# Kernel tuning notes

Hardware: AMD Instinct MI355X
Metric: run time of the kernel (lower is better)

The kernel has to match this reference:

```python
import jax, jax.numpy as jnp
import numpy as np

N_NODES = 50000
N_EDGES = 800000
IN_DIM = 128
HID = 128
BN_EPS = 1e-5


def _linear_init(key, fan_in, fan_out):
    kw, kb = jax.random.split(key)
    bound = 1.0 / np.sqrt(fan_in)
    w = jax.random.uniform(kw, (fan_in, fan_out), minval=-bound, maxval=bound, dtype=jnp.float32)
    b = jax.random.uniform(kb, (fan_out,), minval=-bound, maxval=bound, dtype=jnp.float32)
    return w, b


def setup_inputs() -> dict:
    key = jax.random.key(0)
    ks = jax.random.split(key, 8)
    x = jax.random.normal(ks[0], (N_NODES, IN_DIM), dtype=jnp.float32)
    edge_index = jax.random.randint(ks[1], (2, N_EDGES), 0, N_NODES, dtype=jnp.int32)
    # GIN layer 0 MLP: Linear(IN_DIM,HID) -> ReLU -> Linear(HID,HID)
    w0a, b0a = _linear_init(ks[2], IN_DIM, HID)
    w0b, b0b = _linear_init(ks[3], HID, HID)
    # GIN layer 1 MLP
    w1a, b1a = _linear_init(ks[4], HID, HID)
    w1b, b1b = _linear_init(ks[5], HID, HID)
    # encoder BatchNorm affine params (torch init: gamma=1, beta=0)
    bn_gamma = jnp.ones((HID,), jnp.float32)
    bn_beta = jnp.zeros((HID,), jnp.float32)
    # projection head: Linear(HID,HID) -> BatchNorm -> PReLU -> Dropout
    pw, pb = _linear_init(ks[6], HID, HID)
    pbn_gamma = jnp.ones((HID,), jnp.float32)
    pbn_beta = jnp.zeros((HID,), jnp.float32)
    prelu_a = jnp.asarray(0.25, jnp.float32)  # torch PReLU default init
    return {
        'x': x, 'edge_index': edge_index,
        'w0a': w0a, 'b0a': b0a, 'w0b': w0b, 'b0b': b0b,
        'w1a': w1a, 'b1a': b1a, 'w1b': w1b, 'b1b': b1b,
        'bn_gamma': bn_gamma, 'bn_beta': bn_beta,
        'pw': pw, 'pb': pb, 'pbn_gamma': pbn_gamma, 'pbn_beta': pbn_beta,
        'prelu_a': prelu_a,
    }


def _batch_norm(x, gamma, beta):
    # training-mode BatchNorm1d: biased variance over the node (batch) dim
    mu = jnp.mean(x, axis=0)
    var = jnp.var(x, axis=0)
    return gamma * (x - mu) * jax.lax.rsqrt(var + BN_EPS) + beta


def _gin_conv(z, src, dst, wa, ba, wb, bb):
    # sum-aggregate neighbor features: out[i] = (1+eps)*z[i] + sum_{j->i} z[j], eps=0
    agg = jax.ops.segment_sum(z[src], dst, num_segments=N_NODES)
    h = z + agg
    h = jax.nn.relu(h @ wa + ba)
    return h @ wb + bb


def reference(x, edge_index, w0a, b0a, w0b, b0b, w1a, b1a, w1b, b1b,
              bn_gamma, bn_beta, pw, pb, pbn_gamma, pbn_beta, prelu_a):
    src, dst = edge_index[0], edge_index[1]
    z = x
    z = jax.nn.relu(_gin_conv(z, src, dst, w0a, b0a, w0b, b0b))  # dropout: identity (deterministic)
    z = jax.nn.relu(_gin_conv(z, src, dst, w1a, b1a, w1b, b1b))
    z = _batch_norm(z, bn_gamma, bn_beta)
    p = z @ pw + pb
    p = _batch_norm(p, pbn_gamma, pbn_beta)
    p = jnp.where(p > 0, p, prelu_a * p)  # PReLU, single shared parameter
    return z, p
```

## Files before the change

### kernel.cpp

```cpp
#include <hip/hip_runtime.h>
#include <hip/hip_bf16.h>

#define NN 50000
#define NE 800000
#define HD 128
#define BN_EPS 1e-5f
#define MSTR 132
#define NBUK 782
#define PB 200
#define CHUNK 4000

typedef __attribute__((ext_vector_type(8))) __bf16 bf16x8;
typedef __attribute__((ext_vector_type(4))) __bf16 bf16x4;
typedef __attribute__((ext_vector_type(4))) float floatx4;

__global__ __launch_bounds__(256) void k_prep(const float* __restrict__ W0,
                                              const float* __restrict__ W1,
                                              const float* __restrict__ W2,
                                              const float* __restrict__ W3,
                                              const float* __restrict__ W4,
                                              __bf16* __restrict__ Bh,
                                              __bf16* __restrict__ Bl,
                                              const float* __restrict__ X,
                                              __bf16* __restrict__ Y,
                                              const int* __restrict__ dst,
                                              int* __restrict__ gbtot) {
    __shared__ int h[NBUK];
    const int b = blockIdx.x;
    if (b < 320) {
        const int t = b * 256 + threadIdx.x;
        const int m = t >> 14;
        const int rem = t & 16383;
        const int n = rem >> 7;
        const int k = rem & 127;
        const float* W = (m == 0) ? W0 : (m == 1) ? W1 : (m == 2) ? W2 : (m == 3) ? W3 : W4;
        const float w = W[k * HD + n];
        const __bf16 hi = (__bf16)w;
        const int ct = n >> 4, lm = n & 15;
        const int ks = k >> 5, lq = (k & 31) >> 3, j = k & 7;
        const int lane = lq * 16 + lm;
        const size_t o = (size_t)m * HD * HD + (size_t)(((ct * 4 + ks) * 64) + lane) * 8 + j;
        Bh[o] = hi;
        Bl[o] = (__bf16)(w - (float)hi);
    } else if (b < 320 + 3125) {
        const int i8 = ((b - 320) * 256 + threadIdx.x) * 8;
        const float4 a = *(const float4*)&X[i8];
        const float4 c = *(const float4*)&X[i8 + 4];
        bf16x8 o;
        o[0] = (__bf16)a.x; o[1] = (__bf16)a.y; o[2] = (__bf16)a.z; o[3] = (__bf16)a.w;
        o[4] = (__bf16)c.x; o[5] = (__bf16)c.y; o[6] = (__bf16)c.z; o[7] = (__bf16)c.w;
        *(bf16x8*)&Y[i8] = o;
    } else {
        for (int i = threadIdx.x; i < NBUK; i += 256) h[i] = 0;
        __syncthreads();
        const int e0 = (b - (320 + 3125)) * CHUNK;
        for (int i = threadIdx.x; i < CHUNK; i += 256)
            atomicAdd(&h[dst[e0 + i] >> 6], 1);
        __syncthreads();
        for (int i = threadIdx.x; i < NBUK; i += 256) {
            const int v = h[i];
            if (v) atomicAdd(&gbtot[i], v);
        }
    }
}

__global__ __launch_bounds__(256) void k_bscan(const int* __restrict__ gbtot,
                                               int* __restrict__ bbase,
                                               int* __restrict__ gcur,
                                               int* __restrict__ rowptr) {
    __shared__ int sh[256];
    const int t = threadIdx.x;
    int v[4];
    int s = 0;
#pragma unroll
    for (int j = 0; j < 4; ++j) {
        const int idx = t * 4 + j;
        v[j] = (idx < NBUK) ? gbtot[idx] : 0;
        s += v[j];
    }
    sh[t] = s;
    __syncthreads();
#pragma unroll
    for (int st = 1; st < 256; st <<= 1) {
        int add = (t >= st) ? sh[t - st] : 0;
        __syncthreads();
        sh[t] += add;
        __syncthreads();
    }
    int run = sh[t] - s;
#pragma unroll
    for (int j = 0; j < 4; ++j) {
        const int idx = t * 4 + j;
        if (idx < NBUK) { bbase[idx] = run; gcur[idx] = run; }
        run += v[j];
    }
    if (t == 255) bbase[NBUK] = run;
    if (t == 0) rowptr[NN] = NE;
}

__global__ __launch_bounds__(256) void k_bscatter(const int* __restrict__ src,
                                                  const int* __restrict__ dst,
                                                  int* __restrict__ gcur,
                                                  unsigned* __restrict__ pairs) {
    __shared__ int h[NBUK];
    __shared__ int cur[NBUK];
    for (int i = threadIdx.x; i < NBUK; i += 256) h[i] = 0;
    __syncthreads();
    const int e0 = blockIdx.x * CHUNK;
    for (int i = threadIdx.x; i < CHUNK; i += 256)
        atomicAdd(&h[dst[e0 + i] >> 6], 1);
    __syncthreads();
    for (int i = threadIdx.x; i < NBUK; i += 256) {
        const int v = h[i];
        if (v) cur[i] = atomicAdd(&gcur[i], v);
    }
    __syncthreads();
    for (int i = threadIdx.x; i < CHUNK; i += 256) {
        const int d = dst[e0 + i];
        const int pos = atomicAdd(&cur[d >> 6], 1);
        pairs[pos] = ((unsigned)(d & 63) << 17) | (unsigned)src[e0 + i];
    }
}

__global__ __launch_bounds__(256) void k_csrfin(const unsigned* __restrict__ pairs,
                                                const int* __restrict__ bbase,
                                                int* __restrict__ rowptr,
                                                int* __restrict__ esrc) {
    __shared__ int cnt[64], lof[64], cur[64];
    const int b = blockIdx.x;
    const int s = bbase[b], e = bbase[b + 1];
    const int tid = threadIdx.x;
    if (tid < 64) cnt[tid] = 0;
    __syncthreads();
    for (int i = s + tid; i < e; i += 256)
        atomicAdd(&cnt[pairs[i] >> 17], 1);
    __syncthreads();
    if (tid == 0) {
        int r = 0;
#pragma unroll
        for (int j = 0; j < 64; ++j) { lof[j] = r; cur[j] = r; r += cnt[j]; }
    }
    __syncthreads();
    if (tid < 64) {
        const int node = b * 64 + tid;
        if (node < NN) rowptr[node] = s + lof[tid];
    }
    for (int i = s + tid; i < e; i += 256) {
        const unsigned p = pairs[i];
        const int pos = atomicAdd(&cur[p >> 17], 1);
        esrc[s + pos] = (int)(p & 0x1FFFFu);
    }
}

__device__ __forceinline__ void split8(const float4 a, const float4 b,
                                       bf16x8& hi, bf16x8& lo) {
    hi[0] = (__bf16)a.x; lo[0] = (__bf16)(a.x - (float)hi[0]);
    hi[1] = (__bf16)a.y; lo[1] = (__bf16)(a.y - (float)hi[1]);
    hi[2] = (__bf16)a.z; lo[2] = (__bf16)(a.z - (float)hi[2]);
    hi[3] = (__bf16)a.w; lo[3] = (__bf16)(a.w - (float)hi[3]);
    hi[4] = (__bf16)b.x; lo[4] = (__bf16)(b.x - (float)hi[4]);
    hi[5] = (__bf16)b.y; lo[5] = (__bf16)(b.y - (float)hi[5]);
    hi[6] = (__bf16)b.z; lo[6] = (__bf16)(b.z - (float)hi[6]);
    hi[7] = (__bf16)b.w; lo[7] = (__bf16)(b.w - (float)hi[7]);
}

__device__ __forceinline__ void addb8(float4& a, float4& b, const bf16x8 v) {
    a.x += (float)v[0]; a.y += (float)v[1]; a.z += (float)v[2]; a.w += (float)v[3];
    b.x += (float)v[4]; b.y += (float)v[5]; b.z += (float)v[6]; b.w += (float)v[7];
}

__global__ __launch_bounds__(256) void k_aggb(const __bf16* __restrict__ Z,
                                              const int* __restrict__ rowptr,
                                              const int* __restrict__ esrc,
                                              float* __restrict__ H) {
    const int g = threadIdx.x >> 4;
    const int lg = threadIdx.x & 15;
    const int node = blockIdx.x * 16 + g;
    const int cb = lg * 8;
    const int start = rowptr[node], end = rowptr[node + 1];
    float4 a = {0.f, 0.f, 0.f, 0.f}, b = {0.f, 0.f, 0.f, 0.f};
    addb8(a, b, *(const bf16x8*)&Z[(size_t)node * HD + cb]);
    int k = start;
    for (; k + 16 <= end; k += 16) {
        int s[16];
#pragma unroll
        for (int j = 0; j < 16; ++j) s[j] = esrc[k + j];
        bf16x8 v[16];
#pragma unroll
        for (int j = 0; j < 16; ++j) v[j] = *(const bf16x8*)&Z[(size_t)s[j] * HD + cb];
#pragma unroll
        for (int j = 0; j < 16; ++j) addb8(a, b, v[j]);
    }
    for (; k + 4 <= end; k += 4) {
        const int s0 = esrc[k + 0], s1 = esrc[k + 1];
        const int s2 = esrc[k + 2], s3 = esrc[k + 3];
        const bf16x8 v0 = *(const bf16x8*)&Z[(size_t)s0 * HD + cb];
        const bf16x8 v1 = *(const bf16x8*)&Z[(size_t)s1 * HD + cb];
        const bf16x8 v2 = *(const bf16x8*)&Z[(size_t)s2 * HD + cb];
        const bf16x8 v3 = *(const bf16x8*)&Z[(size_t)s3 * HD + cb];
        addb8(a, b, v0); addb8(a, b, v1); addb8(a, b, v2); addb8(a, b, v3);
    }
    for (; k < end; ++k) {
        const int s = esrc[k];
        addb8(a, b, *(const bf16x8*)&Z[(size_t)s * HD + cb]);
    }
    *(float4*)&H[(size_t)node * HD + cb] = a;
    *(float4*)&H[(size_t)node * HD + cb + 4] = b;
}

struct StageRegs { bf16x8 v[4]; };

__device__ __forceinline__ void stage_load(StageRegs& s, const __bf16* __restrict__ Bh,
                                           const __bf16* __restrict__ Bl,
                                           int ks, int wid, int lane) {
#pragma unroll
    for (int i = 0; i < 4; ++i) {
        const int chunk = wid * 4 + i;
        const int ct = chunk & 7;
        const __bf16* base = (chunk < 8) ? Bh : Bl;
        s.v[i] = *(const bf16x8*)&base[(size_t)(((ct * 4 + ks) * 64) + lane) * 8];
    }
}
__device__ __forceinline__ void stage_write(const StageRegs& s, __bf16* Bb,
                                            int wid, int lane) {
#pragma unroll
    for (int i = 0; i < 4; ++i) {
        const int chunk = wid * 4 + i;
        *(bf16x8*)&Bb[chunk * 512 + lane * 8] = s.v[i];
    }
}

__device__ __forceinline__ void mfma_pass_lds(floatx4 (&acc)[8], const bf16x8 ah,
                                              const bf16x8 al, const __bf16* Bb,
                                              int lane) {
    bf16x8 bh[8], bl[8];
#pragma unroll
    for (int ct = 0; ct < 8; ++ct) {
        bh[ct] = *(const bf16x8*)&Bb[ct * 512 + lane * 8];
        bl[ct] = *(const bf16x8*)&Bb[(8 + ct) * 512 + lane * 8];
    }
    __builtin_amdgcn_sched_barrier(0);
#pragma unroll
    for (int ct = 0; ct < 8; ++ct) {
        acc[ct] = __builtin_amdgcn_mfma_f32_16x16x32_bf16(al, bh[ct], acc[ct], 0, 0, 0);
        acc[ct] = __builtin_amdgcn_mfma_f32_16x16x32_bf16(ah, bl[ct], acc[ct], 0, 0, 0);
        acc[ct] = __builtin_amdgcn_mfma_f32_16x16x32_bf16(ah, bh[ct], acc[ct], 0, 0, 0);
    }
}

template <int STATS, int OUT16>
__global__ __launch_bounds__(256) void k_mlp(const float* __restrict__ A,
                                             const __bf16* __restrict__ Bh1,
                                             const __bf16* __restrict__ Bl1,
                                             const float* __restrict__ b1,
                                             const __bf16* __restrict__ Bh2,
                                             const __bf16* __restrict__ Bl2,
                                             const float* __restrict__ b2,
                                             float* __restrict__ C,
                                             __bf16* __restrict__ C16,
                                             float* __restrict__ pstat) {
    __shared__ float mid[4][16 * MSTR];
    __shared__ __bf16 Bb[2][16 * 512];
    __shared__ float ssum[128], ssq[128];
    const int tid = threadIdx.x;
    const int wid = tid >> 6, lane = tid & 63;
    const int lq = lane >> 4, lm = lane & 15;
    if (STATS && tid < 128) { ssum[tid] = 0.f; ssq[tid] = 0.f; }
    const int rowbase = blockIdx.x * 64 + wid * 16;
    const int r0 = min(rowbase + lm, NN - 1);
    float* m = &mid[wid][0];

    bf16x8 ahv[4], alv[4];
    {
        float4 av[8];
#pragma unroll
        for (int ks = 0; ks < 4; ++ks) {
            const int kk = ks * 32 + lq * 8;
            av[ks * 2 + 0] = *(const float4*)&A[(size_t)r0 * HD + kk];
            av[ks * 2 + 1] = *(const float4*)&A[(size_t)r0 * HD + kk + 4];
        }
#pragma unroll
        for (int ks = 0; ks < 4; ++ks)
            split8(av[ks * 2], av[ks * 2 + 1], ahv[ks], alv[ks]);
    }
    {
        StageRegs s;
        stage_load(s, Bh1, Bl1, 0, wid, lane);
        stage_write(s, &Bb[0][0], wid, lane);
    }
    __syncthreads();

    floatx4 acc[8];
#pragma unroll
    for (int j = 0; j < 8; ++j) acc[j] = (floatx4){0.f, 0.f, 0.f, 0.f};

#pragma unroll
    for (int p = 0; p < 8; ++p) {
        StageRegs s;
        if (p < 7) {
            const int pn = p + 1;
            stage_load(s, (pn < 4) ? Bh1 : Bh2, (pn < 4) ? Bl1 : Bl2, pn & 3, wid, lane);
        }
        bf16x8 ah, al;
        if (p < 4) { ah = ahv[p]; al = alv[p]; }
        else {
            const int kk = (p & 3) * 32 + lq * 8;
            const float4 aa = *(const float4*)&m[lm * MSTR + kk];
            const float4 ab = *(const float4*)&m[lm * MSTR + kk + 4];
            split8(aa, ab, ah, al);
        }
        mfma_pass_lds(acc, ah, al, &Bb[p & 1][0], lane);
        if (p == 3) {
#pragma unroll
            for (int ct = 0; ct < 8; ++ct) {
                const int col = ct * 16 + lm;
                const float bcol = b1[col];
#pragma unroll
                for (int r = 0; r < 4; ++r)
                    m[(lq * 4 + r) * MSTR + col] = fmaxf(acc[ct][r] + bcol, 0.f);
            }
#pragma unroll
            for (int j = 0; j < 8; ++j) acc[j] = (floatx4){0.f, 0.f, 0.f, 0.f};
        }
        if (p < 7) stage_write(s, &Bb[(p + 1) & 1][0], wid, lane);
        __syncthreads();
    }
#pragma unroll
    for (int ct = 0; ct < 8; ++ct) {
        const int col = ct * 16 + lm;
        const float bcol = b2[col];
#pragma unroll
        for (int r = 0; r < 4; ++r)
            m[(lq * 4 + r) * MSTR + col] = fmaxf(acc[ct][r] + bcol, 0.f);
    }
    float s0 = 0.f, s1 = 0.f, s2 = 0.f, s3 = 0.f;
    float q0 = 0.f, q1 = 0.f, q2 = 0.f, q3 = 0.f;
    const int c0 = (lane * 4) & 127;
#pragma unroll
    for (int p = 0; p < 8; ++p) {
        const int idx = p * 256 + lane * 4;
        const int r = idx >> 7;
        const float4 v = *(const float4*)&m[r * MSTR + c0];
        const int row = rowbase + r;
        if (row < NN) {
            if (OUT16) {
                bf16x4 o;
                o[0] = (__bf16)v.x; o[1] = (__bf16)v.y;
                o[2] = (__bf16)v.z; o[3] = (__bf16)v.w;
                *(bf16x4*)&C16[(size_t)row * HD + c0] = o;
            } else {
                *(float4*)&C[(size_t)row * HD + c0] = v;
            }
            if (STATS) {
                s0 += v.x; q0 = fmaf(v.x, v.x, q0);
                s1 += v.y; q1 = fmaf(v.y, v.y, q1);
                s2 += v.z; q2 = fmaf(v.z, v.z, q2);
                s3 += v.w; q3 = fmaf(v.w, v.w, q3);
            }
        }
    }
    if (STATS) {
        s0 += __shfl_xor(s0, 32); q0 += __shfl_xor(q0, 32);
        s1 += __shfl_xor(s1, 32); q1 += __shfl_xor(q1, 32);
        s2 += __shfl_xor(s2, 32); q2 += __shfl_xor(q2, 32);
        s3 += __shfl_xor(s3, 32); q3 += __shfl_xor(q3, 32);
        if (lane < 32) {
            atomicAdd(&ssum[c0 + 0], s0); atomicAdd(&ssq[c0 + 0], q0);
            atomicAdd(&ssum[c0 + 1], s1); atomicAdd(&ssq[c0 + 1], q1);
            atomicAdd(&ssum[c0 + 2], s2); atomicAdd(&ssq[c0 + 2], q2);
            atomicAdd(&ssum[c0 + 3], s3); atomicAdd(&ssq[c0 + 3], q3);
        }
        __syncthreads();
        if (tid < 128) {
            pstat[(size_t)blockIdx.x * 256 + tid] = ssum[tid];
            pstat[(size_t)blockIdx.x * 256 + 128 + tid] = ssq[tid];
        }
    }
}

__global__ __launch_bounds__(256) void k_proj(const float* __restrict__ Z2,
                                              const float* __restrict__ pb2a,
                                              const float* __restrict__ gamma,
                                              const float* __restrict__ beta,
                                              float* __restrict__ Zout,
                                              const __bf16* __restrict__ Bh,
                                              const __bf16* __restrict__ Bl,
                                              const float* __restrict__ bias,
                                              float* __restrict__ C,
                                              float* __restrict__ pstat) {
    __shared__ union {
        __bf16 bb[2][16 * 512];
        float tb[4][16 * MSTR];
    } u;
    __shared__ float ssum[128], ssq[128];
    __shared__ float scs[128], shs[128];
    const int tid = threadIdx.x;
    const int wid = tid >> 6, lane = tid & 63;
    const int lq = lane >> 4, lm = lane & 15;
    if (tid < 128) {
        ssum[tid] = 0.f; ssq[tid] = 0.f;
        float s = 0.f, q = 0.f;
        for (int b = 0; b < 64; ++b) {
            s += pb2a[b * 256 + tid];
            q += pb2a[b * 256 + 128 + tid];
        }
        const float mean = s * (1.f / NN);
        const float var = q * (1.f / NN) - mean * mean;
        const float sc = gamma[tid] * rsqrtf(var + BN_EPS);
        scs[tid] = sc;
        shs[tid] = beta[tid] - mean * sc;
    }
    __syncthreads();
    const int rowbase = blockIdx.x * 64 + wid * 16;
    const int r0 = min(rowbase + lm, NN - 1);
    const bool rowok = (rowbase + lm) < NN;
    float* m = &u.tb[wid][0];

    bf16x8 ahv[4], alv[4];
#pragma unroll
    for (int ks = 0; ks < 4; ++ks) {
        const int kk = ks * 32 + lq * 8;
        const float4 za = *(const float4*)&Z2[(size_t)r0 * HD + kk];
        const float4 zb = *(const float4*)&Z2[(size_t)r0 * HD + kk + 4];
        const float4 sca = *(const float4*)&scs[kk];
        const float4 scb = *(const float4*)&scs[kk + 4];
        const float4 sha = *(const float4*)&shs[kk];
        const float4 shb = *(const float4*)&shs[kk + 4];
        float4 aa, ab;
        aa.x = fmaf(za.x, sca.x, sha.x); aa.y = fmaf(za.y, sca.y, sha.y);
        aa.z = fmaf(za.z, sca.z, sha.z); aa.w = fmaf(za.w, sca.w, sha.w);
        ab.x = fmaf(zb.x, scb.x, shb.x); ab.y = fmaf(zb.y, scb.y, shb.y);
        ab.z = fmaf(zb.z, scb.z, shb.z); ab.w = fmaf(zb.w, scb.w, shb.w);
        if (rowok) {
            *(float4*)&Zout[(size_t)r0 * HD + kk] = aa;
            *(float4*)&Zout[(size_t)r0 * HD + kk + 4] = ab;
        }
        split8(aa, ab, ahv[ks], alv[ks]);
    }
    {
        StageRegs s;
        stage_load(s, Bh, Bl, 0, wid, lane);
        stage_write(s, &u.bb[0][0], wid, lane);
    }
    __syncthreads();

    floatx4 acc[8];
#pragma unroll
    for (int j = 0; j < 8; ++j) acc[j] = (floatx4){0.f, 0.f, 0.f, 0.f};
#pragma unroll
    for (int p = 0; p < 4; ++p) {
        StageRegs s;
        if (p < 3) stage_load(s, Bh, Bl, p + 1, wid, lane);
        mfma_pass_lds(acc, ahv[p], alv[p], &u.bb[p & 1][0], lane);
        if (p < 3) stage_write(s, &u.bb[(p + 1) & 1][0], wid, lane);
        __syncthreads();
    }
#pragma unroll
    for (int ct = 0; ct < 8; ++ct) {
        const int col = ct * 16 + lm;
        const float bcol = bias[col];
#pragma unroll
        for (int r = 0; r < 4; ++r)
            m[(lq * 4 + r) * MSTR + col] = acc[ct][r] + bcol;
    }
    float s0 = 0.f, s1 = 0.f, s2 = 0.f, s3 = 0.f;
    float q0 = 0.f, q1 = 0.f, q2 = 0.f, q3 = 0.f;
    const int c0 = (lane * 4) & 127;
#pragma unroll
    for (int p = 0; p < 8; ++p) {
        const int idx = p * 256 + lane * 4;
        const int r = idx >> 7;
        const float4 v = *(const float4*)&m[r * MSTR + c0];
        const int row = rowbase + r;
        if (row < NN) {
            *(float4*)&C[(size_t)row * HD + c0] = v;
            s0 += v.x; q0 = fmaf(v.x, v.x, q0);
            s1 += v.y; q1 = fmaf(v.y, v.y, q1);
            s2 += v.z; q2 = fmaf(v.z, v.z, q2);
            s3 += v.w; q3 = fmaf(v.w, v.w, q3);
        }
    }
    s0 += __shfl_xor(s0, 32); q0 += __shfl_xor(q0, 32);
    s1 += __shfl_xor(s1, 32); q1 += __shfl_xor(q1, 32);
    s2 += __shfl_xor(s2, 32); q2 += __shfl_xor(q2, 32);
    s3 += __shfl_xor(s3, 32); q3 += __shfl_xor(q3, 32);
    if (lane < 32) {
        atomicAdd(&ssum[c0 + 0], s0); atomicAdd(&ssq[c0 + 0], q0);
        atomicAdd(&ssum[c0 + 1], s1); atomicAdd(&ssq[c0 + 1], q1);
        atomicAdd(&ssum[c0 + 2], s2); atomicAdd(&ssq[c0 + 2], q2);
        atomicAdd(&ssum[c0 + 3], s3); atomicAdd(&ssq[c0 + 3], q3);
    }
    __syncthreads();
    if (tid < 128) {
        pstat[(size_t)blockIdx.x * 256 + tid] = ssum[tid];
        pstat[(size_t)blockIdx.x * 256 + 128 + tid] = ssq[tid];
    }
}

__global__ __launch_bounds__(256) void k_sred(const float* __restrict__ ps, int nblk,
                                              float* __restrict__ out) {
    const int j = threadIdx.x;
    float acc = 0.f;
    for (int r = blockIdx.x; r < nblk; r += 64)
        acc += ps[(size_t)r * 256 + j];
    out[blockIdx.x * 256 + j] = acc;
}

__global__ void k_bnfin(const float* __restrict__ pb2,
                        const float* __restrict__ gamma, const float* __restrict__ beta,
                        float* __restrict__ scale, float* __restrict__ shift) {
    const int c = threadIdx.x;
    float s = 0.f, q = 0.f;
    for (int b = 0; b < 64; ++b) {
        s += pb2[b * 256 + c];
        q += pb2[b * 256 + 128 + c];
    }
    const float mean = s * (1.f / NN);
    const float var = q * (1.f / NN) - mean * mean;
    const float sc = gamma[c] * rsqrtf(var + BN_EPS);
    scale[c] = sc;
    shift[c] = beta[c] - mean * sc;
}

__global__ void k_bnapply(const float* __restrict__ X, const float* __restrict__ scale,
                          const float* __restrict__ shift, float* __restrict__ Y,
                          const float* __restrict__ pa) {
    const int i4 = (blockIdx.x * 256 + threadIdx.x) * 4;
    const int c = i4 & 127;
    const float4 sc = *(const float4*)&scale[c];
    const float4 sh = *(const float4*)&shift[c];
    const float4 v = *(const float4*)&X[i4];
    float4 y;
    y.x = fmaf(v.x, sc.x, sh.x);
    y.y = fmaf(v.y, sc.y, sh.y);
    y.z = fmaf(v.z, sc.z, sh.z);
    y.w = fmaf(v.w, sc.w, sh.w);
    const float a = pa[0];
    if (y.x < 0.f) y.x *= a;
    if (y.y < 0.f) y.y *= a;
    if (y.z < 0.f) y.z *= a;
    if (y.w < 0.f) y.w *= a;
    *(float4*)&Y[i4] = y;
}

extern "C" void kernel_launch(void* const* d_in, const int* in_sizes, int n_in,
                              void* d_out, int out_size, void* d_ws, size_t ws_size,
                              hipStream_t stream) {
    const float* x = (const float*)d_in[0];
    const int* ei = (const int*)d_in[1];
    const float* w0a = (const float*)d_in[2];
    const float* b0a = (const float*)d_in[3];
    const float* w0b = (const float*)d_in[4];
    const float* b0b = (const float*)d_in[5];
    const float* w1a = (const float*)d_in[6];
    const float* b1a = (const float*)d_in[7];
    const float* w1b = (const float*)d_in[8];
    const float* b1b = (const float*)d_in[9];
    const float* bng = (const float*)d_in[10];
    const float* bnb = (const float*)d_in[11];
    const float* pw  = (const float*)d_in[12];
    const float* pb  = (const float*)d_in[13];
    const float* pbng = (const float*)d_in[14];
    const float* pbnb = (const float*)d_in[15];
    const float* pa = (const float*)d_in[16];

    float* outZ = (float*)d_out;
    float* outP = outZ + (size_t)NN * HD;

    float* ws = (float*)d_ws;
    float* bufH = ws;
    float* st = bufH + (size_t)NN * HD;
    int* rowptr = (int*)(st + 1024);
    int* esrc = rowptr + NN + 64;
    int* gbtot = esrc + NE;
    int* bbase = gbtot + 800;
    int* gcur = bbase + 800;
    __bf16* wth = (__bf16*)(gcur + 800);
    __bf16* wtl = wth + 5 * HD * HD;
    float* ps1 = (float*)(wtl + 5 * HD * HD);
    float* pb2a = ps1 + 800 * 256;
    float* ps2 = pb2a + 64 * 256;
    float* pb2b = ps2 + 800 * 256;

    __bf16* xb  = (__bf16*)bufH;
    __bf16* z1b = xb + (size_t)NN * HD;
    unsigned* pairs = (unsigned*)z1b;
    float* Hbuf = outP;

    const int* srcv = ei;
    const int* dstv = ei + NE;

    const int ELV = (NN * HD) / (256 * 4);
    const int GB = (NN + 63) / 64;
    const int AB = NN / 16;
    const int PREPB = 320 + 3125 + PB;

    hipMemsetAsync(gbtot, 0, 800 * sizeof(int), stream);
    k_prep<<<PREPB, 256, 0, stream>>>(w0a, w0b, w1a, w1b, pw, wth, wtl,
                                      x, xb, dstv, gbtot);

    k_bscan<<<1, 256, 0, stream>>>(gbtot, bbase, gcur, rowptr);
    k_bscatter<<<PB, 256, 0, stream>>>(srcv, dstv, gcur, pairs);
    k_csrfin<<<NBUK, 256, 0, stream>>>(pairs, bbase, rowptr, esrc);

    k_aggb<<<AB, 256, 0, stream>>>(xb, rowptr, esrc, Hbuf);
    k_mlp<0, 1><<<GB, 256, 0, stream>>>(Hbuf,
                                        wth + 0 * HD * HD, wtl + 0 * HD * HD, b0a,
                                        wth + 1 * HD * HD, wtl + 1 * HD * HD, b0b,
                                        nullptr, z1b, nullptr);

    k_aggb<<<AB, 256, 0, stream>>>(z1b, rowptr, esrc, Hbuf);
    k_mlp<1, 0><<<GB, 256, 0, stream>>>(Hbuf,
                                        wth + 2 * HD * HD, wtl + 2 * HD * HD, b1a,
                                        wth + 3 * HD * HD, wtl + 3 * HD * HD, b1b,
                                        outP, nullptr, ps1);

    k_sred<<<64, 256, 0, stream>>>(ps1, GB, pb2a);
    k_proj<<<GB, 256, 0, stream>>>(outP, pb2a, bng, bnb, outZ,
                                   wth + 4 * HD * HD, wtl + 4 * HD * HD, pb,
                                   outP, ps2);

    k_sred<<<64, 256, 0, stream>>>(ps2, GB, pb2b);
    k_bnfin<<<1, 128, 0, stream>>>(pb2b, pbng, pbnb, st + 768, st + 896);
    k_bnapply<<<ELV, 256, 0, stream>>>(outP, st + 768, st + 896, outP, pa);
}
```

Measured before the change: 311.1 us.

## Fuse BN stat reductions into consumer kernels via ticket-based in-kernel gates

Removes the separate k_sred and k_bnfin launches by having the first 64 blocks of k_proj and k_ptail, ordered by an atomic ticket, do the partial-statistics reduction and publish completion through a global counter. Other blocks spin-wait on that counter. Meanwhile they prefetch their Z rows and weight tiles, or their X element, so the reduction overlaps with loads. The aim is to cut launch overhead and serialization. The tail kernel merges bn-finalize and apply with a second gate, which relies on all ticket-holding blocks being resident at once to avoid deadlock.

```diff
diff --git a/kernel.cpp b/kernel.cpp
--- a/kernel.cpp
+++ b/kernel.cpp
@@ -9,6 +9,7 @@
 #define NBUK 782
 #define PB 200
 #define CHUNK 4000
+#define GBLK 782
 
 typedef __attribute__((ext_vector_type(8))) __bf16 bf16x8;
 typedef __attribute__((ext_vector_type(4))) __bf16 bf16x4;
@@ -378,8 +379,24 @@
     }
 }
 
+__device__ __forceinline__ int claim_ticket(int* t) {
+    __shared__ int tk;
+    if (threadIdx.x == 0)
+        tk = __hip_atomic_fetch_add(t, 1, __ATOMIC_RELAXED, __HIP_MEMORY_SCOPE_AGENT);
+    __syncthreads();
+    return tk;
+}
+__device__ __forceinline__ void gate_wait(int* c, int target) {
+    if (threadIdx.x == 0)
+        while (__hip_atomic_load(c, __ATOMIC_ACQUIRE, __HIP_MEMORY_SCOPE_AGENT) < target)
+            __builtin_amdgcn_s_sleep(8);
+    __syncthreads();
+}
+
 __global__ __launch_bounds__(256) void k_proj(const float* __restrict__ Z2,
-                                              const float* __restrict__ pb2a,
+                                              const float* __restrict__ ps1,
+                                              float* __restrict__ pb2a,
+                                              int* __restrict__ ctr,
                                               const float* __restrict__ gamma,
                                               const float* __restrict__ beta,
                                               float* __restrict__ Zout,
@@ -397,8 +414,38 @@
     const int tid = threadIdx.x;
     const int wid = tid >> 6, lane = tid & 63;
     const int lq = lane >> 4, lm = lane & 15;
+
+    const int ticket = claim_ticket(&ctr[0]);
+    if (ticket < 64) {
+        float acc = 0.f;
+        for (int r = ticket; r < GBLK; r += 64)
+            acc += ps1[(size_t)r * 256 + tid];
+        pb2a[ticket * 256 + tid] = acc;
+        __threadfence();
+        __syncthreads();
+        if (tid == 0)
+            __hip_atomic_fetch_add(&ctr[1], 1, __ATOMIC_RELEASE, __HIP_MEMORY_SCOPE_AGENT);
+    }
+    if (tid < 128) { ssum[tid] = 0.f; ssq[tid] = 0.f; }
+    const int rowbase = blockIdx.x * 64 + wid * 16;
+    const int r0 = min(rowbase + lm, NN - 1);
+    const bool rowok = (rowbase + lm) < NN;
+    float* m = &u.tb[wid][0];
+
+    float4 zv[8];
+#pragma unroll
+    for (int ks = 0; ks < 4; ++ks) {
+        const int kk = ks * 32 + lq * 8;
+        zv[ks * 2 + 0] = *(const float4*)&Z2[(size_t)r0 * HD + kk];
+        zv[ks * 2 + 1] = *(const float4*)&Z2[(size_t)r0 * HD + kk + 4];
+    }
+    {
+        StageRegs s;
+        stage_load(s, Bh, Bl, 0, wid, lane);
+        stage_write(s, &u.bb[0][0], wid, lane);
+    }
+    gate_wait(&ctr[1], 64);
     if (tid < 128) {
-        ssum[tid] = 0.f; ssq[tid] = 0.f;
         float s = 0.f, q = 0.f;
         for (int b = 0; b < 64; ++b) {
             s += pb2a[b * 256 + tid];
@@ -411,17 +458,13 @@
         shs[tid] = beta[tid] - mean * sc;
     }
     __syncthreads();
-    const int rowbase = blockIdx.x * 64 + wid * 16;
-    const int r0 = min(rowbase + lm, NN - 1);
-    const bool rowok = (rowbase + lm) < NN;
-    float* m = &u.tb[wid][0];
 
     bf16x8 ahv[4], alv[4];
 #pragma unroll
     for (int ks = 0; ks < 4; ++ks) {
         const int kk = ks * 32 + lq * 8;
-        const float4 za = *(const float4*)&Z2[(size_t)r0 * HD + kk];
-        const float4 zb = *(const float4*)&Z2[(size_t)r0 * HD + kk + 4];
+        const float4 za = zv[ks * 2 + 0];
+        const float4 zb = zv[ks * 2 + 1];
         const float4 sca = *(const float4*)&scs[kk];
         const float4 scb = *(const float4*)&scs[kk + 4];
         const float4 sha = *(const float4*)&shs[kk];
@@ -437,13 +480,6 @@
         }
         split8(aa, ab, ahv[ks], alv[ks]);
     }
-    {
-        StageRegs s;
-        stage_load(s, Bh, Bl, 0, wid, lane);
-        stage_write(s, &u.bb[0][0], wid, lane);
-    }
-    __syncthreads();
-
     floatx4 acc[8];
 #pragma unroll
     for (int j = 0; j < 8; ++j) acc[j] = (floatx4){0.f, 0.f, 0.f, 0.f};
@@ -497,50 +533,63 @@
     }
 }
 
-__global__ __launch_bounds__(256) void k_sred(const float* __restrict__ ps, int nblk,
-                                              float* __restrict__ out) {
-    const int j = threadIdx.x;
-    float acc = 0.f;
-    for (int r = blockIdx.x; r < nblk; r += 64)
-        acc += ps[(size_t)r * 256 + j];
-    out[blockIdx.x * 256 + j] = acc;
-}
-
-__global__ void k_bnfin(const float* __restrict__ pb2,
-                        const float* __restrict__ gamma, const float* __restrict__ beta,
-                        float* __restrict__ scale, float* __restrict__ shift) {
-    const int c = threadIdx.x;
-    float s = 0.f, q = 0.f;
-    for (int b = 0; b < 64; ++b) {
-        s += pb2[b * 256 + c];
-        q += pb2[b * 256 + 128 + c];
-    }
-    const float mean = s * (1.f / NN);
-    const float var = q * (1.f / NN) - mean * mean;
-    const float sc = gamma[c] * rsqrtf(var + BN_EPS);
-    scale[c] = sc;
-    shift[c] = beta[c] - mean * sc;
-}
-
-__global__ void k_bnapply(const float* __restrict__ X, const float* __restrict__ scale,
-                          const float* __restrict__ shift, float* __restrict__ Y,
-                          const float* __restrict__ pa) {
-    const int i4 = (blockIdx.x * 256 + threadIdx.x) * 4;
+__global__ __launch_bounds__(256) void k_ptail(const float* __restrict__ ps2,
+                                               float* __restrict__ pb2b,
+                                               int* __restrict__ ctr,
+                                               const float* __restrict__ gamma,
+                                               const float* __restrict__ beta,
+                                               float* __restrict__ scale,
+                                               float* __restrict__ shift,
+                                               float* __restrict__ X,
+                                               const float* __restrict__ pa) {
+    const int tid = threadIdx.x;
+    const int ticket = claim_ticket(&ctr[2]);
+    if (ticket < 64) {
+        float acc = 0.f;
+        for (int r = ticket; r < GBLK; r += 64)
+            acc += ps2[(size_t)r * 256 + tid];
+        pb2b[ticket * 256 + tid] = acc;
+        __threadfence();
+        __syncthreads();
+        if (tid == 0)
+            __hip_atomic_fetch_add(&ctr[3], 1, __ATOMIC_RELEASE, __HIP_MEMORY_SCOPE_AGENT);
+    }
+    const int i4 = (blockIdx.x * 256 + tid) * 4;
+    const float4 v = *(const float4*)&X[i4];
+    const float a = pa[0];
+    if (ticket == 0) {
+        gate_wait(&ctr[3], 64);
+        if (tid < 128) {
+            float s = 0.f, q = 0.f;
+            for (int b = 0; b < 64; ++b) {
+                s += pb2b[b * 256 + tid];
+                q += pb2b[b * 256 + 128 + tid];
+            }
+            const float mean = s * (1.f / NN);
+            const float var = q * (1.f / NN) - mean * mean;
+            const float sc = gamma[tid] * rsqrtf(var + BN_EPS);
+            scale[tid] = sc;
+            shift[tid] = beta[tid] - mean * sc;
+        }
+        __threadfence();
+        __syncthreads();
+        if (tid == 0)
+            __hip_atomic_fetch_add(&ctr[4], 1, __ATOMIC_RELEASE, __HIP_MEMORY_SCOPE_AGENT);
+    }
+    gate_wait(&ctr[4], 1);
     const int c = i4 & 127;
     const float4 sc = *(const float4*)&scale[c];
     const float4 sh = *(const float4*)&shift[c];
-    const float4 v = *(const float4*)&X[i4];
     float4 y;
     y.x = fmaf(v.x, sc.x, sh.x);
     y.y = fmaf(v.y, sc.y, sh.y);
     y.z = fmaf(v.z, sc.z, sh.z);
     y.w = fmaf(v.w, sc.w, sh.w);
-    const float a = pa[0];
     if (y.x < 0.f) y.x *= a;
     if (y.y < 0.f) y.y *= a;
     if (y.z < 0.f) y.z *= a;
     if (y.w < 0.f) y.w *= a;
-    *(float4*)&Y[i4] = y;
+    *(float4*)&X[i4] = y;
 }
 
 extern "C" void kernel_launch(void* const* d_in, const int* in_sizes, int n_in,
@@ -575,7 +624,8 @@
     int* gbtot = esrc + NE;
     int* bbase = gbtot + 800;
     int* gcur = bbase + 800;
-    __bf16* wth = (__bf16*)(gcur + 800);
+    int* ctr = gcur + 800;
+    __bf16* wth = (__bf16*)(ctr + 16);
     __bf16* wtl = wth + 5 * HD * HD;
     float* ps1 = (float*)(wtl + 5 * HD * HD);
     float* pb2a = ps1 + 800 * 256;
@@ -591,11 +641,11 @@
     const int* dstv = ei + NE;
 
     const int ELV = (NN * HD) / (256 * 4);
-    const int GB = (NN + 63) / 64;
+    const int GB = GBLK;
     const int AB = NN / 16;
     const int PREPB = 320 + 3125 + PB;
 
-    hipMemsetAsync(gbtot, 0, 800 * sizeof(int), stream);
+    hipMemsetAsync(gbtot, 0, 2416 * sizeof(int), stream);
     k_prep<<<PREPB, 256, 0, stream>>>(w0a, w0b, w1a, w1b, pw, wth, wtl,
                                       x, xb, dstv, gbtot);
 
@@ -615,12 +665,10 @@
                                         wth + 3 * HD * HD, wtl + 3 * HD * HD, b1b,
                                         outP, nullptr, ps1);
 
-    k_sred<<<64, 256, 0, stream>>>(ps1, GB, pb2a);
-    k_proj<<<GB, 256, 0, stream>>>(outP, pb2a, bng, bnb, outZ,
+    k_proj<<<GB, 256, 0, stream>>>(outP, ps1, pb2a, ctr, bng, bnb, outZ,
                                    wth + 4 * HD * HD, wtl + 4 * HD * HD, pb,
                                    outP, ps2);
 
-    k_sred<<<64, 256, 0, stream>>>(ps2, GB, pb2b);
-    k_bnfin<<<1, 128, 0, stream>>>(pb2b, pbng, pbnb, st + 768, st + 896);
-    k_bnapply<<<ELV, 256, 0, stream>>>(outP, st + 768, st + 896, outP, pa);
-}
+    k_ptail<<<ELV, 256, 0, stream>>>(ps2, pb2b, ctr, pbng, pbnb,
+                                     st + 768, st + 896, outP, pa);
+}
```

Measured after the change: 812.8 us. 161% more time.
